# Optimization experiments

Hardware: AMD Instinct MI355X
Metric: run time of the kernel (lower is better)

The kernel has to match this reference:

```python
import jax, jax.numpy as jnp
import numpy as np

N = 131072
IN, HID, OUT = 128, 256, 64
NUM_TASKS = 16
NUM_COPIES = 4
NUM_LAYERS = 3


def setup_inputs() -> dict:
    key = jax.random.key(0)
    ks = jax.random.split(key, 10)
    inputs = jax.random.normal(ks[0], (N, IN), dtype=jnp.float32)
    task_indices = jax.random.randint(ks[1], (N,), 0, NUM_TASKS, dtype=jnp.int32)
    copy_maps = jax.random.randint(ks[2], (NUM_LAYERS, NUM_TASKS), 0, NUM_COPIES, dtype=jnp.int32)
    # per-copy Linear weights, Kaiming-ish scale 1/sqrt(fan_in)
    W0 = jax.random.normal(ks[3], (NUM_COPIES, IN, HID), dtype=jnp.float32) / np.sqrt(IN)
    b0 = jax.random.normal(ks[4], (NUM_COPIES, HID), dtype=jnp.float32) * 0.01
    W1 = jax.random.normal(ks[5], (NUM_COPIES, HID, HID), dtype=jnp.float32) / np.sqrt(HID)
    b1 = jax.random.normal(ks[6], (NUM_COPIES, HID), dtype=jnp.float32) * 0.01
    W2 = jax.random.normal(ks[7], (NUM_COPIES, HID, OUT), dtype=jnp.float32) / np.sqrt(HID)
    b2 = jax.random.normal(ks[8], (NUM_COPIES, OUT), dtype=jnp.float32) * 0.01
    return {"inputs": inputs, "task_indices": task_indices, "copy_maps": copy_maps,
            "W0": W0, "b0": b0, "W1": W1, "b1": b1, "W2": W2, "b2": b2}


def _routed_layer(x, W, b, copy_idx, apply_tanh):
    # x: [N, d_in], W: [C, d_in, d_out], b: [C, d_out], copy_idx: [N]
    # Each token goes through exactly one copy's Linear. Equivalent to the
    # torch sort->per-copy-forward->unsort, expressed as masked accumulation
    # over the small fixed set of copies (avoids data-dependent shapes).
    y = jnp.zeros((x.shape[0], W.shape[2]), dtype=x.dtype)
    for c in range(W.shape[0]):
        mask = (copy_idx == c).astype(x.dtype)[:, None]  # [N, 1]
        y = y + mask * (x @ W[c] + b[c])
    return jnp.tanh(y) if apply_tanh else y


def reference(inputs, task_indices, copy_maps, W0, b0, W1, b1, W2, b2):
    x = inputs
    Ws = (W0, W1, W2)
    bs = (b0, b1, b2)
    for layer in range(NUM_LAYERS):
        copy_idx = copy_maps[layer][task_indices]  # [N] task->copy routing
        x = _routed_layer(x, Ws[layer], bs[layer], copy_idx,
                          apply_tanh=(layer != NUM_LAYERS - 1))
    return x
```

## Files before the change

### kernel.cpp

```cpp
#include <hip/hip_runtime.h>

#define N_TOK 131072
#define TILE 64
#define NT_MAX 2064
#define XS 136
#define HS 264
#define SCR_S 68

typedef __attribute__((ext_vector_type(8))) short s8v;
typedef __attribute__((ext_vector_type(4))) float f4v;
typedef unsigned short ushort_t;

__device__ __forceinline__ unsigned short f2bf(float x) {
    union { float f; unsigned u; } v; v.f = x;
    unsigned r = v.u + 0x7fffu + ((v.u >> 16) & 1u);
    return (unsigned short)(r >> 16);
}

__device__ __forceinline__ float tanh_fast(float x) {
    float e = __expf(2.0f * x);
    return 1.0f - 2.0f / (e + 1.0f);
}

__global__ void prep_kernel(const float* __restrict__ W0, const float* __restrict__ W1,
                            const float* __restrict__ W2,
                            ushort_t* __restrict__ W0p, ushort_t* __restrict__ W1p,
                            ushort_t* __restrict__ W2p) {
    int f = blockIdx.x * 256 + threadIdx.x;
    const float* src; ushort_t* dst; int K, N;
    if (f < 16384)      { src = W0; dst = W0p; K = 128; N = 256; }
    else if (f < 49152) { src = W1; dst = W1p; K = 256; N = 256; f -= 16384; }
    else if (f < 57344) { src = W2; dst = W2p; K = 256; N = 64;  f -= 49152; }
    else return;
    int fpc = (N >> 4) * (K >> 5) * 64;
    int c = f / fpc, r = f % fpc;
    int lane = r & 63;
    int kt = (r >> 6) % (K >> 5);
    int ntile = (r >> 6) / (K >> 5);
    int n = ntile * 16 + (lane & 15);
    int kbase = kt * 32 + (lane >> 4) * 8;
    const float* s = src + (size_t)c * K * N + (size_t)kbase * N + n;
    s8v pk;
#pragma unroll
    for (int j = 0; j < 8; j++) pk[j] = (short)f2bf(s[(size_t)j * N]);
    *reinterpret_cast<s8v*>(dst + ((size_t)(c * fpc + r) << 3)) = pk;
}

__global__ void hist_kernel(const int* __restrict__ task, int* __restrict__ blockCounts) {
    __shared__ int cnt[16];
    int t = threadIdx.x;
    if (t < 16) cnt[t] = 0;
    __syncthreads();
    int base = blockIdx.x * 2048 + t;
#pragma unroll
    for (int i = 0; i < 8; i++) atomicAdd(&cnt[task[base + i * 256]], 1);
    __syncthreads();
    if (t < 16) blockCounts[blockIdx.x * 16 + t] = cnt[t];
}

__global__ void scan_kernel(const int* __restrict__ blockCounts, int* __restrict__ cur,
                            int* __restrict__ tileTask, int* __restrict__ nT) {
    __shared__ int cnt[16];
    __shared__ int tbase[17];
    int t = threadIdx.x;
    if (t < 16) {
        int s = 0;
#pragma unroll
        for (int b = 0; b < 64; b++) s += blockCounts[b * 16 + t];
        cnt[t] = s;
    }
    __syncthreads();
    if (t == 0) {
        int tok = 0, tile = 0;
        for (int k = 0; k < 16; k++) {
            cur[k] = tok;
            int ntk = (cnt[k] + TILE - 1) / TILE;
            tbase[k] = tile;
            tok += ntk * TILE;
            tile += ntk;
        }
        tbase[16] = tile;
        nT[0] = tile;
    }
    __syncthreads();
    for (int i = t; i < NT_MAX; i += 256) {
        int tk = 0;
        if (i < tbase[16]) {
#pragma unroll
            for (int k = 0; k < 16; k++) if (i >= tbase[k]) tk = k;
        }
        tileTask[i] = tk;
    }
}

__global__ void scatter_kernel(const int* __restrict__ task, int* __restrict__ cur,
                               int* __restrict__ perm) {
    __shared__ int cnt[16];
    __shared__ int basesh[16];
    int t = threadIdx.x;
    if (t < 16) cnt[t] = 0;
    __syncthreads();
    int tk[8], my[8];
#pragma unroll
    for (int i = 0; i < 8; i++) {
        int idx = blockIdx.x * 2048 + i * 256 + t;
        tk[i] = task[idx];
        my[i] = atomicAdd(&cnt[tk[i]], 1);
    }
    __syncthreads();
    if (t < 16) basesh[t] = atomicAdd(&cur[t], cnt[t]);
    __syncthreads();
#pragma unroll
    for (int i = 0; i < 8; i++) {
        int idx = blockIdx.x * 2048 + i * 256 + t;
        perm[basesh[tk[i]] + my[i]] = idx;
    }
}

__launch_bounds__(512, 4)
__global__ void mlp_kernel(const float* __restrict__ x_in,
                           const int* __restrict__ cmap,
                           const float* __restrict__ b0,
                           const float* __restrict__ b1,
                           const float* __restrict__ b2,
                           const ushort_t* __restrict__ W0p,
                           const ushort_t* __restrict__ W1p,
                           const ushort_t* __restrict__ W2p,
                           const int* __restrict__ tileTask,
                           const int* __restrict__ nTp,
                           const int* __restrict__ perm,
                           float* __restrict__ out) {
    __shared__ __align__(16) ushort_t bufA[TILE * HS];
    __shared__ __align__(16) ushort_t bufB[TILE * HS];
    __shared__ int toks[TILE];

    int b = blockIdx.x;
    if (b >= nTp[0]) return;
    int t = threadIdx.x;
    int task = tileTask[b];
    int c0 = cmap[task], c1 = cmap[16 + task], c2 = cmap[32 + task];
    if (t < TILE) toks[t] = perm[b * TILE + t];
    __syncthreads();

    {
        int r = t >> 3, q = t & 7;
        unsigned tok = (unsigned)toks[r];
        float4 v[4];
        if (tok < (unsigned)N_TOK) {
            const float4* src = reinterpret_cast<const float4*>(x_in) + (size_t)tok * 32 + q * 4;
#pragma unroll
            for (int i = 0; i < 4; i++) v[i] = src[i];
        } else {
#pragma unroll
            for (int i = 0; i < 4; i++) v[i] = make_float4(0.f, 0.f, 0.f, 0.f);
        }
        ushort_t* dst = &bufA[r * XS + q * 16];
#pragma unroll
        for (int i = 0; i < 2; i++) {
            float4 va = v[2 * i], vb = v[2 * i + 1];
            s8v pk;
            pk[0] = (short)f2bf(va.x); pk[1] = (short)f2bf(va.y);
            pk[2] = (short)f2bf(va.z); pk[3] = (short)f2bf(va.w);
            pk[4] = (short)f2bf(vb.x); pk[5] = (short)f2bf(vb.y);
            pk[6] = (short)f2bf(vb.z); pk[7] = (short)f2bf(vb.w);
            *reinterpret_cast<s8v*>(dst + i * 8) = pk;
        }
    }
    __syncthreads();

    int w = t >> 6;
    int lane = t & 63;
    int l15 = lane & 15, lq = lane >> 4;

    {
        f4v acc[4][2];
#pragma unroll
        for (int mt = 0; mt < 4; mt++)
#pragma unroll
            for (int nt = 0; nt < 2; nt++) { f4v z = {0.f, 0.f, 0.f, 0.f}; acc[mt][nt] = z; }
        const ushort_t* Wc = W0p + (size_t)c0 * 32768;
#pragma unroll
        for (int kt = 0; kt < 4; kt++) {
            s8v a[4];
#pragma unroll
            for (int mt = 0; mt < 4; mt++)
                a[mt] = *reinterpret_cast<const s8v*>(&bufA[(mt * 16 + l15) * XS + kt * 32 + lq * 8]);
            s8v bb[2];
#pragma unroll
            for (int nt = 0; nt < 2; nt++) {
                int n16 = w * 2 + nt;
                bb[nt] = *reinterpret_cast<const s8v*>(Wc + (((n16 * 4 + kt) * 64 + lane) << 3));
            }
#pragma unroll
            for (int mt = 0; mt < 4; mt++)
#pragma unroll
                for (int nt = 0; nt < 2; nt++)
                    acc[mt][nt] = __builtin_amdgcn_mfma_f32_16x16x32_bf16(a[mt], bb[nt], acc[mt][nt], 0, 0, 0);
        }
        float bias[2];
#pragma unroll
        for (int nt = 0; nt < 2; nt++) bias[nt] = b0[c0 * 256 + w * 32 + nt * 16 + l15];
#pragma unroll
        for (int mt = 0; mt < 4; mt++)
#pragma unroll
            for (int nt = 0; nt < 2; nt++)
#pragma unroll
                for (int rg = 0; rg < 4; rg++) {
                    float v = tanh_fast(acc[mt][nt][rg] + bias[nt]);
                    bufB[(mt * 16 + lq * 4 + rg) * HS + w * 32 + nt * 16 + l15] = f2bf(v);
                }
    }
    __syncthreads();

    {
        f4v acc[4][2];
#pragma unroll
        for (int mt = 0; mt < 4; mt++)
#pragma unroll
            for (int nt = 0; nt < 2; nt++) { f4v z = {0.f, 0.f, 0.f, 0.f}; acc[mt][nt] = z; }
        const ushort_t* Wc = W1p + (size_t)c1 * 65536;
#pragma unroll
        for (int kt = 0; kt < 8; kt++) {
            s8v a[4];
#pragma unroll
            for (int mt = 0; mt < 4; mt++)
                a[mt] = *reinterpret_cast<const s8v*>(&bufB[(mt * 16 + l15) * HS + kt * 32 + lq * 8]);
            s8v bb[2];
#pragma unroll
            for (int nt = 0; nt < 2; nt++) {
                int n16 = w * 2 + nt;
                bb[nt] = *reinterpret_cast<const s8v*>(Wc + (((n16 * 8 + kt) * 64 + lane) << 3));
            }
#pragma unroll
            for (int mt = 0; mt < 4; mt++)
#pragma unroll
                for (int nt = 0; nt < 2; nt++)
                    acc[mt][nt] = __builtin_amdgcn_mfma_f32_16x16x32_bf16(a[mt], bb[nt], acc[mt][nt], 0, 0, 0);
        }
        float bias[2];
#pragma unroll
        for (int nt = 0; nt < 2; nt++) bias[nt] = b1[c1 * 256 + w * 32 + nt * 16 + l15];
#pragma unroll
        for (int mt = 0; mt < 4; mt++)
#pragma unroll
            for (int nt = 0; nt < 2; nt++)
#pragma unroll
                for (int rg = 0; rg < 4; rg++) {
                    float v = tanh_fast(acc[mt][nt][rg] + bias[nt]);
                    bufA[(mt * 16 + lq * 4 + rg) * HS + w * 32 + nt * 16 + l15] = f2bf(v);
                }
    }
    __syncthreads();

    {
        int n16 = w & 3, khalf = w >> 2;
        f4v acc[4];
#pragma unroll
        for (int mt = 0; mt < 4; mt++) { f4v z = {0.f, 0.f, 0.f, 0.f}; acc[mt] = z; }
        const ushort_t* Wc = W2p + (size_t)c2 * 16384;
#pragma unroll
        for (int ki = 0; ki < 4; ki++) {
            int kt = khalf * 4 + ki;
            s8v a[4];
#pragma unroll
            for (int mt = 0; mt < 4; mt++)
                a[mt] = *reinterpret_cast<const s8v*>(&bufA[(mt * 16 + l15) * HS + kt * 32 + lq * 8]);
            s8v bb = *reinterpret_cast<const s8v*>(Wc + (((n16 * 8 + kt) * 64 + lane) << 3));
#pragma unroll
            for (int mt = 0; mt < 4; mt++)
                acc[mt] = __builtin_amdgcn_mfma_f32_16x16x32_bf16(a[mt], bb, acc[mt], 0, 0, 0);
        }
        float* scratch = reinterpret_cast<float*>(bufB);
        if (khalf == 1) {
#pragma unroll
            for (int mt = 0; mt < 4; mt++)
#pragma unroll
                for (int rg = 0; rg < 4; rg++) {
                    int row = mt * 16 + lq * 4 + rg;
                    scratch[row * SCR_S + n16 * 16 + l15] = acc[mt][rg];
                }
        }
        __syncthreads();
        if (khalf == 0) {
            float bias = b2[c2 * 64 + n16 * 16 + l15];
#pragma unroll
            for (int mt = 0; mt < 4; mt++)
#pragma unroll
                for (int rg = 0; rg < 4; rg++) {
                    int row = mt * 16 + lq * 4 + rg;
                    unsigned tok = (unsigned)toks[row];
                    if (tok < (unsigned)N_TOK) {
                        float v = acc[mt][rg] + scratch[row * SCR_S + n16 * 16 + l15] + bias;
                        out[(size_t)tok * 64 + n16 * 16 + l15] = v;
                    }
                }
        }
    }
}

extern "C" void kernel_launch(void* const* d_in, const int* in_sizes, int n_in,
                              void* d_out, int out_size, void* d_ws, size_t ws_size,
                              hipStream_t stream) {
    const float* inputs = (const float*)d_in[0];
    const int*   task   = (const int*)d_in[1];
    const int*   cmap   = (const int*)d_in[2];
    const float* W0     = (const float*)d_in[3];
    const float* b0     = (const float*)d_in[4];
    const float* W1     = (const float*)d_in[5];
    const float* b1     = (const float*)d_in[6];
    const float* W2     = (const float*)d_in[7];
    const float* b2     = (const float*)d_in[8];
    float* out = (float*)d_out;

    char* ws = (char*)d_ws;
    int* blockCounts = (int*)(ws + 0);
    int* cur         = (int*)(ws + 4096);
    int* nT          = (int*)(ws + 4160);
    int* tileTask    = (int*)(ws + 4352);
    int* perm        = (int*)(ws + 12800);
    ushort_t* W0p    = (ushort_t*)(ws + 541696);
    ushort_t* W1p    = (ushort_t*)(ws + 803840);
    ushort_t* W2p    = (ushort_t*)(ws + 1328128);

    prep_kernel<<<224, 256, 0, stream>>>(W0, W1, W2, W0p, W1p, W2p);
    hist_kernel<<<64, 256, 0, stream>>>(task, blockCounts);
    scan_kernel<<<1, 256, 0, stream>>>(blockCounts, cur, tileTask, nT);
    scatter_kernel<<<64, 256, 0, stream>>>(task, cur, perm);
    mlp_kernel<<<NT_MAX, 512, 0, stream>>>(inputs, cmap, b0, b1, b2,
                                           W0p, W1p, W2p, tileTask, nT, perm, out);
}
```

Baseline: 188.7 us.

## Fuse preprocessing kernels and swap MFMA operand roles for vectorized epilogues

Merges weight packing with the task histogram, and merges scan and scatter into one sort kernel where each block computes its own prefix, cutting the launch count from five to three. The MLP kernel now puts weights in the MFMA A operand and tokens in B. Each lane therefore holds four consecutive features per token, which allows 8-byte packed LDS stores of the hidden activations and float4 bias loads and output stores. The last layer no longer splits K with a scratch reduction and an extra barrier. The perm load is folded into the input staging to drop one sync. The risks are different LDS bank-conflict patterns and redundant prefix work in each sort block.

```diff
diff --git a/kernel.cpp b/kernel.cpp
--- a/kernel.cpp
+++ b/kernel.cpp
@@ -5,9 +5,9 @@
 #define NT_MAX 2064
 #define XS 136
 #define HS 264
-#define SCR_S 68
 
 typedef __attribute__((ext_vector_type(8))) short s8v;
+typedef __attribute__((ext_vector_type(4))) short s4v;
 typedef __attribute__((ext_vector_type(4))) float f4v;
 typedef unsigned short ushort_t;
 
@@ -22,98 +22,98 @@
     return 1.0f - 2.0f / (e + 1.0f);
 }
 
-__global__ void prep_kernel(const float* __restrict__ W0, const float* __restrict__ W1,
-                            const float* __restrict__ W2,
-                            ushort_t* __restrict__ W0p, ushort_t* __restrict__ W1p,
-                            ushort_t* __restrict__ W2p) {
-    int f = blockIdx.x * 256 + threadIdx.x;
-    const float* src; ushort_t* dst; int K, N;
-    if (f < 16384)      { src = W0; dst = W0p; K = 128; N = 256; }
-    else if (f < 49152) { src = W1; dst = W1p; K = 256; N = 256; f -= 16384; }
-    else if (f < 57344) { src = W2; dst = W2p; K = 256; N = 64;  f -= 49152; }
-    else return;
-    int fpc = (N >> 4) * (K >> 5) * 64;
-    int c = f / fpc, r = f % fpc;
-    int lane = r & 63;
-    int kt = (r >> 6) % (K >> 5);
-    int ntile = (r >> 6) / (K >> 5);
-    int n = ntile * 16 + (lane & 15);
-    int kbase = kt * 32 + (lane >> 4) * 8;
-    const float* s = src + (size_t)c * K * N + (size_t)kbase * N + n;
-    s8v pk;
-#pragma unroll
-    for (int j = 0; j < 8; j++) pk[j] = (short)f2bf(s[(size_t)j * N]);
-    *reinterpret_cast<s8v*>(dst + ((size_t)(c * fpc + r) << 3)) = pk;
-}
-
-__global__ void hist_kernel(const int* __restrict__ task, int* __restrict__ blockCounts) {
-    __shared__ int cnt[16];
-    int t = threadIdx.x;
-    if (t < 16) cnt[t] = 0;
-    __syncthreads();
-    int base = blockIdx.x * 2048 + t;
-#pragma unroll
-    for (int i = 0; i < 8; i++) atomicAdd(&cnt[task[base + i * 256]], 1);
-    __syncthreads();
-    if (t < 16) blockCounts[blockIdx.x * 16 + t] = cnt[t];
-}
-
-__global__ void scan_kernel(const int* __restrict__ blockCounts, int* __restrict__ cur,
-                            int* __restrict__ tileTask, int* __restrict__ nT) {
-    __shared__ int cnt[16];
-    __shared__ int tbase[17];
-    int t = threadIdx.x;
+__global__ void prep_hist_kernel(const float* __restrict__ W0, const float* __restrict__ W1,
+                                 const float* __restrict__ W2,
+                                 ushort_t* __restrict__ W0p, ushort_t* __restrict__ W1p,
+                                 ushort_t* __restrict__ W2p,
+                                 const int* __restrict__ task, int* __restrict__ blockCounts) {
+    if (blockIdx.x < 224) {
+        int f = blockIdx.x * 256 + threadIdx.x;
+        const float* src; ushort_t* dst; int K, N;
+        if (f < 16384)      { src = W0; dst = W0p; K = 128; N = 256; }
+        else if (f < 49152) { src = W1; dst = W1p; K = 256; N = 256; f -= 16384; }
+        else                { src = W2; dst = W2p; K = 256; N = 64;  f -= 49152; }
+        int fpc = (N >> 4) * (K >> 5) * 64;
+        int c = f / fpc, r = f % fpc;
+        int lane = r & 63;
+        int kt = (r >> 6) % (K >> 5);
+        int ftile = (r >> 6) / (K >> 5);
+        int n = ftile * 16 + (lane & 15);
+        int kbase = kt * 32 + (lane >> 4) * 8;
+        const float* s = src + (size_t)c * K * N + (size_t)kbase * N + n;
+        s8v pk;
+#pragma unroll
+        for (int j = 0; j < 8; j++) pk[j] = (short)f2bf(s[(size_t)j * N]);
+        *reinterpret_cast<s8v*>(dst + ((size_t)(c * fpc + r) << 3)) = pk;
+    } else {
+        __shared__ int cnt[16];
+        int t = threadIdx.x;
+        int hb = blockIdx.x - 224;
+        if (t < 16) cnt[t] = 0;
+        __syncthreads();
+        int base = hb * 2048 + t;
+#pragma unroll
+        for (int i = 0; i < 8; i++) atomicAdd(&cnt[task[base + i * 256]], 1);
+        __syncthreads();
+        if (t < 16) blockCounts[hb * 16 + t] = cnt[t];
+    }
+}
+
+__global__ void sort_kernel(const int* __restrict__ task, const int* __restrict__ blockCounts,
+                            int* __restrict__ tileTask, int* __restrict__ nT,
+                            int* __restrict__ perm) {
+    __shared__ int cntLds[1024];
+    __shared__ int total[16], pref[16], rank[16];
+    __shared__ int tokBase[16], tbase[17];
+    int t = threadIdx.x, b = blockIdx.x;
+    for (int i = t; i < 1024; i += 256) cntLds[i] = blockCounts[i];
+    if (t < 16) rank[t] = 0;
+    __syncthreads();
     if (t < 16) {
-        int s = 0;
-#pragma unroll
-        for (int b = 0; b < 64; b++) s += blockCounts[b * 16 + t];
-        cnt[t] = s;
+        int tot = 0, pf = 0;
+#pragma unroll
+        for (int bb = 0; bb < 64; bb++) {
+            int v = cntLds[bb * 16 + t];
+            tot += v;
+            if (bb < b) pf += v;
+        }
+        total[t] = tot; pref[t] = pf;
     }
     __syncthreads();
     if (t == 0) {
         int tok = 0, tile = 0;
         for (int k = 0; k < 16; k++) {
-            cur[k] = tok;
-            int ntk = (cnt[k] + TILE - 1) / TILE;
+            tokBase[k] = tok;
             tbase[k] = tile;
+            int ntk = (total[k] + TILE - 1) / TILE;
             tok += ntk * TILE;
             tile += ntk;
         }
         tbase[16] = tile;
-        nT[0] = tile;
-    }
-    __syncthreads();
-    for (int i = t; i < NT_MAX; i += 256) {
-        int tk = 0;
-        if (i < tbase[16]) {
-#pragma unroll
-            for (int k = 0; k < 16; k++) if (i >= tbase[k]) tk = k;
-        }
-        tileTask[i] = tk;
-    }
-}
-
-__global__ void scatter_kernel(const int* __restrict__ task, int* __restrict__ cur,
-                               int* __restrict__ perm) {
-    __shared__ int cnt[16];
-    __shared__ int basesh[16];
-    int t = threadIdx.x;
-    if (t < 16) cnt[t] = 0;
-    __syncthreads();
+        if (b == 0) nT[0] = tile;
+    }
+    __syncthreads();
+    if (b == 0) {
+        for (int i = t; i < NT_MAX; i += 256) {
+            int tk = 0;
+            if (i < tbase[16]) {
+#pragma unroll
+                for (int k = 0; k < 16; k++) if (i >= tbase[k]) tk = k;
+            }
+            tileTask[i] = tk;
+        }
+    }
     int tk[8], my[8];
 #pragma unroll
     for (int i = 0; i < 8; i++) {
-        int idx = blockIdx.x * 2048 + i * 256 + t;
+        int idx = b * 2048 + i * 256 + t;
         tk[i] = task[idx];
-        my[i] = atomicAdd(&cnt[tk[i]], 1);
-    }
-    __syncthreads();
-    if (t < 16) basesh[t] = atomicAdd(&cur[t], cnt[t]);
-    __syncthreads();
+        my[i] = atomicAdd(&rank[tk[i]], 1);
+    }
 #pragma unroll
     for (int i = 0; i < 8; i++) {
-        int idx = blockIdx.x * 2048 + i * 256 + t;
-        perm[basesh[tk[i]] + my[i]] = idx;
+        int idx = b * 2048 + i * 256 + t;
+        perm[tokBase[tk[i]] + pref[tk[i]] + my[i]] = idx;
     }
 }
 
@@ -139,14 +139,13 @@
     int t = threadIdx.x;
     int task = tileTask[b];
     int c0 = cmap[task], c1 = cmap[16 + task], c2 = cmap[32 + task];
-    if (t < TILE) toks[t] = perm[b * TILE + t];
-    __syncthreads();
 
     {
         int r = t >> 3, q = t & 7;
-        unsigned tok = (unsigned)toks[r];
+        int tok = perm[b * TILE + r];
+        if (q == 0) toks[r] = tok;
         float4 v[4];
-        if (tok < (unsigned)N_TOK) {
+        if ((unsigned)tok < (unsigned)N_TOK) {
             const float4* src = reinterpret_cast<const float4*>(x_in) + (size_t)tok * 32 + q * 4;
 #pragma unroll
             for (int i = 0; i < 4; i++) v[i] = src[i];
@@ -173,127 +172,116 @@
     int l15 = lane & 15, lq = lane >> 4;
 
     {
-        f4v acc[4][2];
-#pragma unroll
-        for (int mt = 0; mt < 4; mt++)
-#pragma unroll
-            for (int nt = 0; nt < 2; nt++) { f4v z = {0.f, 0.f, 0.f, 0.f}; acc[mt][nt] = z; }
+        f4v acc[2][4];
+#pragma unroll
+        for (int mi = 0; mi < 2; mi++)
+#pragma unroll
+            for (int nt = 0; nt < 4; nt++) { f4v z = {0.f, 0.f, 0.f, 0.f}; acc[mi][nt] = z; }
         const ushort_t* Wc = W0p + (size_t)c0 * 32768;
 #pragma unroll
         for (int kt = 0; kt < 4; kt++) {
-            s8v a[4];
-#pragma unroll
-            for (int mt = 0; mt < 4; mt++)
-                a[mt] = *reinterpret_cast<const s8v*>(&bufA[(mt * 16 + l15) * XS + kt * 32 + lq * 8]);
-            s8v bb[2];
-#pragma unroll
-            for (int nt = 0; nt < 2; nt++) {
-                int n16 = w * 2 + nt;
-                bb[nt] = *reinterpret_cast<const s8v*>(Wc + (((n16 * 4 + kt) * 64 + lane) << 3));
-            }
-#pragma unroll
-            for (int mt = 0; mt < 4; mt++)
-#pragma unroll
-                for (int nt = 0; nt < 2; nt++)
-                    acc[mt][nt] = __builtin_amdgcn_mfma_f32_16x16x32_bf16(a[mt], bb[nt], acc[mt][nt], 0, 0, 0);
-        }
-        float bias[2];
-#pragma unroll
-        for (int nt = 0; nt < 2; nt++) bias[nt] = b0[c0 * 256 + w * 32 + nt * 16 + l15];
-#pragma unroll
-        for (int mt = 0; mt < 4; mt++)
-#pragma unroll
-            for (int nt = 0; nt < 2; nt++)
-#pragma unroll
-                for (int rg = 0; rg < 4; rg++) {
-                    float v = tanh_fast(acc[mt][nt][rg] + bias[nt]);
-                    bufB[(mt * 16 + lq * 4 + rg) * HS + w * 32 + nt * 16 + l15] = f2bf(v);
-                }
+            s8v xb[4];
+#pragma unroll
+            for (int nt = 0; nt < 4; nt++)
+                xb[nt] = *reinterpret_cast<const s8v*>(&bufA[(nt * 16 + l15) * XS + kt * 32 + lq * 8]);
+            s8v wa[2];
+#pragma unroll
+            for (int mi = 0; mi < 2; mi++)
+                wa[mi] = *reinterpret_cast<const s8v*>(Wc + ((((2 * w + mi) * 4 + kt) * 64 + lane) << 3));
+#pragma unroll
+            for (int mi = 0; mi < 2; mi++)
+#pragma unroll
+                for (int nt = 0; nt < 4; nt++)
+                    acc[mi][nt] = __builtin_amdgcn_mfma_f32_16x16x32_bf16(wa[mi], xb[nt], acc[mi][nt], 0, 0, 0);
+        }
+#pragma unroll
+        for (int mi = 0; mi < 2; mi++) {
+            int fbase = (2 * w + mi) * 16 + lq * 4;
+            float4 bv = *reinterpret_cast<const float4*>(b0 + c0 * 256 + fbase);
+            float br[4] = {bv.x, bv.y, bv.z, bv.w};
+#pragma unroll
+            for (int nt = 0; nt < 4; nt++) {
+                s4v pk;
+#pragma unroll
+                for (int rg = 0; rg < 4; rg++)
+                    pk[rg] = (short)f2bf(tanh_fast(acc[mi][nt][rg] + br[rg]));
+                *reinterpret_cast<s4v*>(&bufB[(nt * 16 + l15) * HS + fbase]) = pk;
+            }
+        }
     }
     __syncthreads();
 
     {
-        f4v acc[4][2];
-#pragma unroll
-        for (int mt = 0; mt < 4; mt++)
-#pragma unroll
-            for (int nt = 0; nt < 2; nt++) { f4v z = {0.f, 0.f, 0.f, 0.f}; acc[mt][nt] = z; }
+        f4v acc[2][4];
+#pragma unroll
+        for (int mi = 0; mi < 2; mi++)
+#pragma unroll
+            for (int nt = 0; nt < 4; nt++) { f4v z = {0.f, 0.f, 0.f, 0.f}; acc[mi][nt] = z; }
         const ushort_t* Wc = W1p + (size_t)c1 * 65536;
 #pragma unroll
         for (int kt = 0; kt < 8; kt++) {
-            s8v a[4];
-#pragma unroll
-            for (int mt = 0; mt < 4; mt++)
-                a[mt] = *reinterpret_cast<const s8v*>(&bufB[(mt * 16 + l15) * HS + kt * 32 + lq * 8]);
-            s8v bb[2];
-#pragma unroll
-            for (int nt = 0; nt < 2; nt++) {
-                int n16 = w * 2 + nt;
-                bb[nt] = *reinterpret_cast<const s8v*>(Wc + (((n16 * 8 + kt) * 64 + lane) << 3));
-            }
-#pragma unroll
-            for (int mt = 0; mt < 4; mt++)
-#pragma unroll
-                for (int nt = 0; nt < 2; nt++)
-                    acc[mt][nt] = __builtin_amdgcn_mfma_f32_16x16x32_bf16(a[mt], bb[nt], acc[mt][nt], 0, 0, 0);
-        }
-        float bias[2];
-#pragma unroll
-        for (int nt = 0; nt < 2; nt++) bias[nt] = b1[c1 * 256 + w * 32 + nt * 16 + l15];
-#pragma unroll
-        for (int mt = 0; mt < 4; mt++)
-#pragma unroll
-            for (int nt = 0; nt < 2; nt++)
-#pragma unroll
-                for (int rg = 0; rg < 4; rg++) {
-                    float v = tanh_fast(acc[mt][nt][rg] + bias[nt]);
-                    bufA[(mt * 16 + lq * 4 + rg) * HS + w * 32 + nt * 16 + l15] = f2bf(v);
-                }
+            s8v xb[4];
+#pragma unroll
+            for (int nt = 0; nt < 4; nt++)
+                xb[nt] = *reinterpret_cast<const s8v*>(&bufB[(nt * 16 + l15) * HS + kt * 32 + lq * 8]);
+            s8v wa[2];
+#pragma unroll
+            for (int mi = 0; mi < 2; mi++)
+                wa[mi] = *reinterpret_cast<const s8v*>(Wc + ((((2 * w + mi) * 8 + kt) * 64 + lane) << 3));
+#pragma unroll
+            for (int mi = 0; mi < 2; mi++)
+#pragma unroll
+                for (int nt = 0; nt < 4; nt++)
+                    acc[mi][nt] = __builtin_amdgcn_mfma_f32_16x16x32_bf16(wa[mi], xb[nt], acc[mi][nt], 0, 0, 0);
+        }
+#pragma unroll
+        for (int mi = 0; mi < 2; mi++) {
+            int fbase = (2 * w + mi) * 16 + lq * 4;
+            float4 bv = *reinterpret_cast<const float4*>(b1 + c1 * 256 + fbase);
+            float br[4] = {bv.x, bv.y, bv.z, bv.w};
+#pragma unroll
+            for (int nt = 0; nt < 4; nt++) {
+                s4v pk;
+#pragma unroll
+                for (int rg = 0; rg < 4; rg++)
+                    pk[rg] = (short)f2bf(tanh_fast(acc[mi][nt][rg] + br[rg]));
+                *reinterpret_cast<s4v*>(&bufA[(nt * 16 + l15) * HS + fbase]) = pk;
+            }
+        }
     }
     __syncthreads();
 
     {
-        int n16 = w & 3, khalf = w >> 2;
-        f4v acc[4];
-#pragma unroll
-        for (int mt = 0; mt < 4; mt++) { f4v z = {0.f, 0.f, 0.f, 0.f}; acc[mt] = z; }
+        int mti = w & 3, half = w >> 2;
+        f4v acc2[2];
+#pragma unroll
+        for (int j = 0; j < 2; j++) { f4v z = {0.f, 0.f, 0.f, 0.f}; acc2[j] = z; }
         const ushort_t* Wc = W2p + (size_t)c2 * 16384;
 #pragma unroll
-        for (int ki = 0; ki < 4; ki++) {
-            int kt = khalf * 4 + ki;
-            s8v a[4];
-#pragma unroll
-            for (int mt = 0; mt < 4; mt++)
-                a[mt] = *reinterpret_cast<const s8v*>(&bufA[(mt * 16 + l15) * HS + kt * 32 + lq * 8]);
-            s8v bb = *reinterpret_cast<const s8v*>(Wc + (((n16 * 8 + kt) * 64 + lane) << 3));
-#pragma unroll
-            for (int mt = 0; mt < 4; mt++)
-                acc[mt] = __builtin_amdgcn_mfma_f32_16x16x32_bf16(a[mt], bb, acc[mt], 0, 0, 0);
-        }
-        float* scratch = reinterpret_cast<float*>(bufB);
-        if (khalf == 1) {
-#pragma unroll
-            for (int mt = 0; mt < 4; mt++)
-#pragma unroll
-                for (int rg = 0; rg < 4; rg++) {
-                    int row = mt * 16 + lq * 4 + rg;
-                    scratch[row * SCR_S + n16 * 16 + l15] = acc[mt][rg];
-                }
-        }
-        __syncthreads();
-        if (khalf == 0) {
-            float bias = b2[c2 * 64 + n16 * 16 + l15];
-#pragma unroll
-            for (int mt = 0; mt < 4; mt++)
-#pragma unroll
-                for (int rg = 0; rg < 4; rg++) {
-                    int row = mt * 16 + lq * 4 + rg;
-                    unsigned tok = (unsigned)toks[row];
-                    if (tok < (unsigned)N_TOK) {
-                        float v = acc[mt][rg] + scratch[row * SCR_S + n16 * 16 + l15] + bias;
-                        out[(size_t)tok * 64 + n16 * 16 + l15] = v;
-                    }
-                }
+        for (int kt = 0; kt < 8; kt++) {
+            s8v xb[2];
+#pragma unroll
+            for (int j = 0; j < 2; j++) {
+                int nt = half * 2 + j;
+                xb[j] = *reinterpret_cast<const s8v*>(&bufA[(nt * 16 + l15) * HS + kt * 32 + lq * 8]);
+            }
+            s8v wa = *reinterpret_cast<const s8v*>(Wc + (((mti * 8 + kt) * 64 + lane) << 3));
+#pragma unroll
+            for (int j = 0; j < 2; j++)
+                acc2[j] = __builtin_amdgcn_mfma_f32_16x16x32_bf16(wa, xb[j], acc2[j], 0, 0, 0);
+        }
+        int fbase = mti * 16 + lq * 4;
+        float4 bv = *reinterpret_cast<const float4*>(b2 + c2 * 64 + fbase);
+#pragma unroll
+        for (int j = 0; j < 2; j++) {
+            int row = (half * 2 + j) * 16 + l15;
+            int tok = toks[row];
+            if ((unsigned)tok < (unsigned)N_TOK) {
+                float4 o;
+                o.x = acc2[j][0] + bv.x; o.y = acc2[j][1] + bv.y;
+                o.z = acc2[j][2] + bv.z; o.w = acc2[j][3] + bv.w;
+                *reinterpret_cast<float4*>(out + (size_t)tok * 64 + fbase) = o;
+            }
         }
     }
 }
@@ -314,18 +302,15 @@
 
     char* ws = (char*)d_ws;
     int* blockCounts = (int*)(ws + 0);
-    int* cur         = (int*)(ws + 4096);
-    int* nT          = (int*)(ws + 4160);
-    int* tileTask    = (int*)(ws + 4352);
-    int* perm        = (int*)(ws + 12800);
-    ushort_t* W0p    = (ushort_t*)(ws + 541696);
-    ushort_t* W1p    = (ushort_t*)(ws + 803840);
-    ushort_t* W2p    = (ushort_t*)(ws + 1328128);
-
-    prep_kernel<<<224, 256, 0, stream>>>(W0, W1, W2, W0p, W1p, W2p);
-    hist_kernel<<<64, 256, 0, stream>>>(task, blockCounts);
-    scan_kernel<<<1, 256, 0, stream>>>(blockCounts, cur, tileTask, nT);
-    scatter_kernel<<<64, 256, 0, stream>>>(task, cur, perm);
+    int* nT          = (int*)(ws + 4096);
+    int* tileTask    = (int*)(ws + 4160);
+    int* perm        = (int*)(ws + 12416);
+    ushort_t* W0p    = (ushort_t*)(ws + 540800);
+    ushort_t* W1p    = (ushort_t*)(ws + 802944);
+    ushort_t* W2p    = (ushort_t*)(ws + 1327232);
+
+    prep_hist_kernel<<<288, 256, 0, stream>>>(W0, W1, W2, W0p, W1p, W2p, task, blockCounts);
+    sort_kernel<<<64, 256, 0, stream>>>(task, blockCounts, tileTask, nT, perm);
     mlp_kernel<<<NT_MAX, 512, 0, stream>>>(inputs, cmap, b0, b1, b2,
                                            W0p, W1p, W2p, tileTask, nT, perm, out);
 }
```

Result: faster. 179.3 us (-5.0%).
